# Optimization experiments

Hardware: AMD Instinct MI355X
Metric: run time of the kernel (lower is better)

## Reference

```python
import jax, jax.numpy as jnp
import numpy as np
import math

VOCAB = 128000
D_MODEL = 1024
CUTOFFS = [20000, 60000, VOCAB]  # cluster boundaries (last = vocab_size)
B, S = 8, 4096


def setup_inputs() -> dict:
    key = jax.random.key(0)
    ks = jax.random.split(key, 6)
    input_ids = jax.random.randint(ks[0], (B, S), 0, VOCAB)
    # cluster 0: ids [0, 20000), dim 1024, padding_idx=0 -> zero row
    emb0 = jax.random.normal(ks[1], (20000, 1024), jnp.float32)
    emb0 = emb0.at[0].set(0.0)
    # cluster 1: ids [20000, 60000), dim 256 (= 1024 // 4**1)
    emb1 = jax.random.normal(ks[2], (40000, 256), jnp.float32)
    # cluster 2: ids [60000, 128000), dim 64 (= 1024 // 4**2)
    emb2 = jax.random.normal(ks[3], (68000, 64), jnp.float32)
    # nn.Linear(emb_dim, d_model, bias=False): weight shape [d_model, emb_dim]
    proj1 = jax.random.normal(ks[4], (1024, 256), jnp.float32) * 0.02
    proj2 = jax.random.normal(ks[5], (1024, 64), jnp.float32) * 0.02
    return {"input_ids": input_ids, "emb0": emb0, "emb1": emb1, "emb2": emb2,
            "proj1": proj1, "proj2": proj2}


def reference(input_ids, emb0, emb1, emb2, proj1, proj2):
    d_model = emb0.shape[1]
    starts = [0, CUTOFFS[0], CUTOFFS[1]]
    ends = CUTOFFS
    tables = [emb0, emb1, emb2]
    projs = [None, proj1, proj2]
    out = jnp.zeros(input_ids.shape + (d_model,), jnp.float32)
    for start, end, tab, proj in zip(starts, ends, tables, projs):
        mask = (input_ids >= start) & (input_ids < end)          # [B,S]
        local = jnp.clip(input_ids - start, 0, tab.shape[0] - 1)  # in-range gather ids
        e = tab[local]                                            # [B,S,emb_dim]
        if proj is not None:
            e = jnp.einsum('bse,de->bsd', e, proj)                # project to d_model
        else:
            # padding_idx=0: row is zero; mask keeps grad out of row 0 too
            e = e * (input_ids != 0)[..., None].astype(e.dtype)
        out = out + jnp.where(mask[..., None], e, 0.0)            # masked scatter
    return out * math.sqrt(d_model)
```

## Files before the change

### kernel.cpp

```cpp
#include <hip/hip_runtime.h>
#include <hip/hip_bf16.h>


typedef __attribute__((ext_vector_type(4))) float        float4v;
typedef __attribute__((ext_vector_type(8))) short        short8;
typedef __attribute__((ext_vector_type(2))) unsigned int uint2v;
typedef __attribute__((ext_vector_type(2))) int          int2v;

#define D_MODEL 1024

__device__ __forceinline__ short f2bf(float x) {
    unsigned u = __builtin_bit_cast(unsigned, x);
    unsigned r = u + 0x7fffu + ((u >> 16) & 1u);
    return (short)(r >> 16);
}

__device__ __forceinline__ uint2v pack4(float4v v) {
    uint2v r;
    r[0] = (unsigned)(unsigned short)f2bf(v[0]) | ((unsigned)(unsigned short)f2bf(v[1]) << 16);
    r[1] = (unsigned)(unsigned short)f2bf(v[2]) | ((unsigned)(unsigned short)f2bf(v[3]) << 16);
    return r;
}

__global__ __launch_bounds__(1024)
void prep_k(const int* __restrict__ ids, int n, int pb,
            int* __restrict__ cnt,
            int2v* __restrict__ l0, int2v* __restrict__ l1, int2v* __restrict__ l2,
            const float* __restrict__ proj1, const float* __restrict__ proj2,
            uint2v* __restrict__ p1bf, uint2v* __restrict__ p2bf)
{
    const int b = blockIdx.x;
    if (b >= pb) {
        int bb = b - pb;
        if (bb < 64) {
            int t = bb * 1024 + threadIdx.x;
            p1bf[t] = pack4(((const float4v*)proj1)[t]);
        } else {
            int t = (bb - 64) * 1024 + threadIdx.x;
            p2bf[t] = pack4(((const float4v*)proj2)[t]);
        }
        return;
    }

    __shared__ int s_wcnt[16][3];
    __shared__ int s_wbase[16][3];
    __shared__ int s_base[3];

    const int tid  = threadIdx.x;
    const int wave = tid >> 6;
    const int lane = tid & 63;
    const int i    = b * 1024 + tid;

    int id = (i < n) ? ids[i] : -1;
    bool is0 = (i < n) && (id < 20000);
    bool is1 = (i < n) && (id >= 20000) && (id < 60000);
    bool is2 = (i < n) && (id >= 60000);
    unsigned long long ltmask = (lane == 0) ? 0ull : (~0ull >> (64 - lane));

    unsigned long long m0 = __ballot(is0);
    unsigned long long m1 = __ballot(is1);
    unsigned long long m2 = __ballot(is2);
    if (lane == 0) {
        s_wcnt[wave][0] = __popcll(m0);
        s_wcnt[wave][1] = __popcll(m1);
        s_wcnt[wave][2] = __popcll(m2);
    }
    __syncthreads();

    if (tid < 3) {
        const int c = tid;
        int run = 0;
#pragma unroll
        for (int w = 0; w < 16; w++) { s_wbase[w][c] = run; run += s_wcnt[w][c]; }
        const int gidx = (c == 0) ? 2 : (c - 1);
        s_base[c] = atomicAdd(&cnt[gidx], run);
    }
    __syncthreads();

    if (is0) l0[s_base[0] + s_wbase[wave][0] + __popcll(m0 & ltmask)] = (int2v){i, id};
    if (is1) l1[s_base[1] + s_wbase[wave][1] + __popcll(m1 & ltmask)] = (int2v){i, id - 20000};
    if (is2) l2[s_base[2] + s_wbase[wave][2] + __popcll(m2 & ltmask)] = (int2v){i, id - 60000};
}

template<int K>
__device__ __forceinline__
void gemm_item(int tile, int dimh,
               const float* __restrict__ table,
               const short* __restrict__ pbf,
               const int2v* __restrict__ list,
               int count,
               float* __restrict__ out,
               int2v* s_tl, short* s_a)
{
    constexpr int PK = K + 8;
    const int m_base = tile * 16;
    const int tid = threadIdx.x;
    if (tid < 16) {
        int m = m_base + tid;
        s_tl[tid] = (m < count) ? list[m] : (int2v){-1, 0};
    }
    __syncthreads();

    {
        const int row = tid >> 4;
        const int c   = tid & 15;
        const float* src = table + (size_t)s_tl[row][1] * K + c * (K / 16);
        short*       dst = s_a + row * PK + c * (K / 16);
        if constexpr (K == 256) {
            const float4v* s4 = (const float4v*)src;
            float4v f0 = s4[0], f1 = s4[1], f2 = s4[2], f3 = s4[3];
            uint2v* d2 = (uint2v*)dst;
            d2[0] = pack4(f0); d2[1] = pack4(f1);
            d2[2] = pack4(f2); d2[3] = pack4(f3);
        } else {
            float4v f0 = *(const float4v*)src;
            *(uint2v*)dst = pack4(f0);
        }
    }
    __syncthreads();

    const int lane = tid & 63;
    const int wave = tid >> 6;
    const int col  = lane & 15;
    const int quad = lane >> 4;
    const int nb   = dimh * 512 + wave * 128;

    const short* arow  = s_a + col * PK + quad * 8;
    const short* bbase = pbf + (size_t)(nb + col) * K + quad * 8;

    float4v acc[8];
#pragma unroll
    for (int i = 0; i < 8; i++) acc[i] = (float4v){0.f, 0.f, 0.f, 0.f};

#pragma unroll
    for (int ks = 0; ks < K; ks += 32) {
        short8 a = *(const short8*)(arow + ks);
#pragma unroll
        for (int nt = 0; nt < 8; nt++) {
            short8 b = *(const short8*)(bbase + (size_t)nt * 16 * K + ks);
            acc[nt] = __builtin_amdgcn_mfma_f32_16x16x32_bf16(a, b, acc[nt], 0, 0, 0);
        }
    }

#pragma unroll
    for (int r = 0; r < 4; r++) {
        int row = quad * 4 + r;
        if (m_base + row < count) {
            float* orow = out + (size_t)s_tl[row][0] * D_MODEL + nb + col;
#pragma unroll
            for (int nt = 0; nt < 8; nt++) orow[nt * 16] = acc[nt][r] * 32.0f;
        }
    }
    __syncthreads();
}

__device__ __forceinline__
void copy_item(int item, const int2v* __restrict__ l0, int count0,
               const float* __restrict__ emb0, float* __restrict__ out)
{
    int r = item * 4 + (threadIdx.x >> 6);
    if (r < count0) {
        int2v tl = l0[r];
        const float4v* src = (const float4v*)(emb0 + (size_t)tl[1] * D_MODEL);
        float4v*       dst = (float4v*)(out + (size_t)tl[0] * D_MODEL);
        int c = threadIdx.x & 63;
        float4v v0 = src[c], v1 = src[c + 64], v2 = src[c + 128], v3 = src[c + 192];
        dst[c]       = v0 * 32.0f;
        dst[c + 64]  = v1 * 32.0f;
        dst[c + 128] = v2 * 32.0f;
        dst[c + 192] = v3 * 32.0f;
    }
}

__global__ __launch_bounds__(256, 5)
void fused_main(const float* __restrict__ emb0,
                const float* __restrict__ emb1,
                const float* __restrict__ emb2,
                const short* __restrict__ p1bf,
                const short* __restrict__ p2bf,
                const int2v* __restrict__ l0,
                const int2v* __restrict__ l1,
                const int2v* __restrict__ l2,
                const int* __restrict__ cnt,
                float* __restrict__ out)
{
    __shared__ int2v s_tl[16];
    __shared__ short s_a[16 * 264];

    const int c1 = cnt[0];
    const int c2 = cnt[1];
    const int c0 = cnt[2];
    const int g1 = ((c1 + 15) >> 4) * 2;
    const int g2 = ((c2 + 15) >> 4) * 2;
    const int tc = (c0 + 3) >> 2;
    const int total = g1 + g2 + tc;

    for (int w = blockIdx.x; w < total; w += gridDim.x) {
        if (w < g1) {
            gemm_item<256>(w >> 1, w & 1, emb1, p1bf, l1, c1, out, s_tl, s_a);
        } else if (w < g1 + g2) {
            int u = w - g1;
            gemm_item<64>(u >> 1, u & 1, emb2, p2bf, l2, c2, out, s_tl, s_a);
        } else {
            copy_item(w - g1 - g2, l0, c0, emb0, out);
        }
    }
}

extern "C" void kernel_launch(void* const* d_in, const int* in_sizes, int n_in,
                              void* d_out, int out_size, void* d_ws, size_t ws_size,
                              hipStream_t stream)
{
    const int*   ids   = (const int*)  d_in[0];
    const float* emb0  = (const float*)d_in[1];
    const float* emb1  = (const float*)d_in[2];
    const float* emb2  = (const float*)d_in[3];
    const float* proj1 = (const float*)d_in[4];
    const float* proj2 = (const float*)d_in[5];
    float*       out   = (float*)d_out;
    const int n = in_sizes[0];

    int*   cnt  = (int*)d_ws;
    int2v* l0   = (int2v*)((char*)d_ws + 256);
    int2v* l1   = l0 + n;
    int2v* l2   = l1 + n;
    size_t poff = (256 + (size_t)3 * n * 8 + 255) & ~(size_t)255;
    short* p1bf = (short*)((char*)d_ws + poff);
    short* p2bf = p1bf + 1024 * 256;

    const int pb = (n + 1023) / 1024;

    hipMemsetAsync(cnt, 0, 4 * sizeof(int), stream);
    prep_k<<<pb + 64 + 16, 1024, 0, stream>>>(ids, n, pb, cnt, l0, l1, l2,
                                              proj1, proj2,
                                              (uint2v*)p1bf, (uint2v*)p2bf);
    fused_main<<<4096, 256, 0, stream>>>(emb0, emb1, emb2,
                                         p1bf, p2bf, l0, l1, l2, cnt, out);
}
```

Before: 289.4 us.

## Enlarge GEMM tiles to 32 rows, pre-swizzle projections, stage stores via LDS

The projection weights are now converted to bf16 in an MFMA-fragment order, so each lane loads one contiguous short8 per B fragment and the loads coalesce. Each 512-thread block now handles a 32-token tile across the full 1024-wide output, so two accumulator sets share every B fragment and the projection weights are re-read less often. Results are transposed through LDS so each row is written with float4 stores instead of scattered scalar stores. The cost is more registers and LDS per block (launch bounds change to 512 threads, 4 blocks) and extra barriers.

```diff
diff --git a/kernel.cpp b/kernel.cpp
--- a/kernel.cpp
+++ b/kernel.cpp
@@ -13,6 +13,13 @@
     unsigned u = __builtin_bit_cast(unsigned, x);
     unsigned r = u + 0x7fffu + ((u >> 16) & 1u);
     return (short)(r >> 16);
+}
+
+__device__ __forceinline__ short8 cvt8(float4v a, float4v b) {
+    short8 r;
+    r[0] = f2bf(a[0]); r[1] = f2bf(a[1]); r[2] = f2bf(a[2]); r[3] = f2bf(a[3]);
+    r[4] = f2bf(b[0]); r[5] = f2bf(b[1]); r[6] = f2bf(b[2]); r[7] = f2bf(b[3]);
+    return r;
 }
 
 __device__ __forceinline__ uint2v pack4(float4v v) {
@@ -27,17 +34,29 @@
             int* __restrict__ cnt,
             int2v* __restrict__ l0, int2v* __restrict__ l1, int2v* __restrict__ l2,
             const float* __restrict__ proj1, const float* __restrict__ proj2,
-            uint2v* __restrict__ p1bf, uint2v* __restrict__ p2bf)
+            short8* __restrict__ p1bf, short8* __restrict__ p2bf)
 {
     const int b = blockIdx.x;
     if (b >= pb) {
         int bb = b - pb;
-        if (bb < 64) {
-            int t = bb * 1024 + threadIdx.x;
-            p1bf[t] = pack4(((const float4v*)proj1)[t]);
+        if (bb < 32) {
+            int t    = bb * 1024 + threadIdx.x;
+            int lane = t & 63;
+            int ks32 = (t >> 6) & 7;
+            int nt   = t >> 9;
+            int nrow = nt * 16 + (lane & 15);
+            int k0   = ks32 * 32 + (lane >> 4) * 8;
+            const float* s = proj1 + nrow * 256 + k0;
+            p1bf[t] = cvt8(*(const float4v*)s, *(const float4v*)(s + 4));
         } else {
-            int t = (bb - 64) * 1024 + threadIdx.x;
-            p2bf[t] = pack4(((const float4v*)proj2)[t]);
+            int t    = (bb - 32) * 1024 + threadIdx.x;
+            int lane = t & 63;
+            int ks32 = (t >> 6) & 1;
+            int nt   = t >> 7;
+            int nrow = nt * 16 + (lane & 15);
+            int k0   = ks32 * 32 + (lane >> 4) * 8;
+            const float* s = proj2 + nrow * 64 + k0;
+            p2bf[t] = cvt8(*(const float4v*)s, *(const float4v*)(s + 4));
         }
         return;
     }
@@ -84,18 +103,19 @@
 
 template<int K>
 __device__ __forceinline__
-void gemm_item(int tile, int dimh,
+void gemm_tile(int tile,
                const float* __restrict__ table,
-               const short* __restrict__ pbf,
+               const short8* __restrict__ pbf,
                const int2v* __restrict__ list,
                int count,
                float* __restrict__ out,
-               int2v* s_tl, short* s_a)
+               int2v* s_tl, short* s_a, float* s_t)
 {
     constexpr int PK = K + 8;
-    const int m_base = tile * 16;
+    constexpr int KS = K / 32;
+    const int m_base = tile * 32;
     const int tid = threadIdx.x;
-    if (tid < 16) {
+    if (tid < 32) {
         int m = m_base + tid;
         s_tl[tid] = (m < count) ? list[m] : (int2v){-1, 0};
     }
@@ -104,7 +124,7 @@
     {
         const int row = tid >> 4;
         const int c   = tid & 15;
-        const float* src = table + (size_t)s_tl[row][1] * K + c * (K / 16);
+        const float* src = s_tl ? table + (size_t)s_tl[row][1] * K + c * (K / 16) : nullptr;
         short*       dst = s_a + row * PK + c * (K / 16);
         if constexpr (K == 256) {
             const float4v* s4 = (const float4v*)src;
@@ -123,32 +143,65 @@
     const int wave = tid >> 6;
     const int col  = lane & 15;
     const int quad = lane >> 4;
-    const int nb   = dimh * 512 + wave * 128;
-
-    const short* arow  = s_a + col * PK + quad * 8;
-    const short* bbase = pbf + (size_t)(nb + col) * K + quad * 8;
-
-    float4v acc[8];
-#pragma unroll
-    for (int i = 0; i < 8; i++) acc[i] = (float4v){0.f, 0.f, 0.f, 0.f};
-
-#pragma unroll
-    for (int ks = 0; ks < K; ks += 32) {
-        short8 a = *(const short8*)(arow + ks);
+
+    const short* arow0 = s_a + col * PK        + quad * 8;
+    const short* arow1 = s_a + (col + 16) * PK + quad * 8;
+
+    float4v acc0[8], acc1[8];
+#pragma unroll
+    for (int i = 0; i < 8; i++) {
+        acc0[i] = (float4v){0.f, 0.f, 0.f, 0.f};
+        acc1[i] = (float4v){0.f, 0.f, 0.f, 0.f};
+    }
+
+#pragma unroll
+    for (int ks32 = 0; ks32 < KS; ks32++) {
+        short8 a0 = *(const short8*)(arow0 + ks32 * 32);
+        short8 a1 = *(const short8*)(arow1 + ks32 * 32);
+        const short8* bp = pbf + ((size_t)(wave * 8) * KS + ks32) * 64 + lane;
 #pragma unroll
         for (int nt = 0; nt < 8; nt++) {
-            short8 b = *(const short8*)(bbase + (size_t)nt * 16 * K + ks);
-            acc[nt] = __builtin_amdgcn_mfma_f32_16x16x32_bf16(a, b, acc[nt], 0, 0, 0);
-        }
-    }
-
-#pragma unroll
-    for (int r = 0; r < 4; r++) {
-        int row = quad * 4 + r;
-        if (m_base + row < count) {
-            float* orow = out + (size_t)s_tl[row][0] * D_MODEL + nb + col;
-#pragma unroll
-            for (int nt = 0; nt < 8; nt++) orow[nt * 16] = acc[nt][r] * 32.0f;
+            short8 b = bp[(size_t)nt * KS * 64];
+            acc0[nt] = __builtin_amdgcn_mfma_f32_16x16x32_bf16(a0, b, acc0[nt], 0, 0, 0);
+            acc1[nt] = __builtin_amdgcn_mfma_f32_16x16x32_bf16(a1, b, acc1[nt], 0, 0, 0);
+        }
+    }
+
+    __syncthreads();
+    float* tsc = s_t + wave * (16 * 132);
+    const int c4 = (lane & 31) * 4;
+    const int half = lane >> 5;
+
+#pragma unroll
+    for (int nt = 0; nt < 8; nt++)
+#pragma unroll
+        for (int r = 0; r < 4; r++)
+            tsc[(quad * 4 + r) * 132 + nt * 16 + col] = acc0[nt][r] * 32.0f;
+    __syncthreads();
+#pragma unroll
+    for (int s = 0; s < 8; s++) {
+        int R = s * 2 + half;
+        float4v v = *(const float4v*)&tsc[R * 132 + c4];
+        if (m_base + R < count) {
+            int tok = s_tl[R][0];
+            *(float4v*)(out + (size_t)tok * D_MODEL + wave * 128 + c4) = v;
+        }
+    }
+    __syncthreads();
+
+#pragma unroll
+    for (int nt = 0; nt < 8; nt++)
+#pragma unroll
+        for (int r = 0; r < 4; r++)
+            tsc[(quad * 4 + r) * 132 + nt * 16 + col] = acc1[nt][r] * 32.0f;
+    __syncthreads();
+#pragma unroll
+    for (int s = 0; s < 8; s++) {
+        int R = s * 2 + half;
+        float4v v = *(const float4v*)&tsc[R * 132 + c4];
+        if (m_base + 16 + R < count) {
+            int tok = s_tl[16 + R][0];
+            *(float4v*)(out + (size_t)tok * D_MODEL + wave * 128 + c4) = v;
         }
     }
     __syncthreads();
@@ -158,7 +211,7 @@
 void copy_item(int item, const int2v* __restrict__ l0, int count0,
                const float* __restrict__ emb0, float* __restrict__ out)
 {
-    int r = item * 4 + (threadIdx.x >> 6);
+    int r = item * 8 + (threadIdx.x >> 6);
     if (r < count0) {
         int2v tl = l0[r];
         const float4v* src = (const float4v*)(emb0 + (size_t)tl[1] * D_MODEL);
@@ -172,37 +225,38 @@
     }
 }
 
-__global__ __launch_bounds__(256, 5)
+__global__ __launch_bounds__(512, 4)
 void fused_main(const float* __restrict__ emb0,
                 const float* __restrict__ emb1,
                 const float* __restrict__ emb2,
-                const short* __restrict__ p1bf,
-                const short* __restrict__ p2bf,
+                const short8* __restrict__ p1bf,
+                const short8* __restrict__ p2bf,
                 const int2v* __restrict__ l0,
                 const int2v* __restrict__ l1,
                 const int2v* __restrict__ l2,
                 const int* __restrict__ cnt,
                 float* __restrict__ out)
 {
-    __shared__ int2v s_tl[16];
-    __shared__ short s_a[16 * 264];
+    __shared__ int2v s_tl[32];
+    __shared__ char  s_buf[8 * 16 * 132 * 4];
+    short* s_a = (short*)s_buf;
+    float* s_t = (float*)s_buf;
 
     const int c1 = cnt[0];
     const int c2 = cnt[1];
     const int c0 = cnt[2];
-    const int g1 = ((c1 + 15) >> 4) * 2;
-    const int g2 = ((c2 + 15) >> 4) * 2;
-    const int tc = (c0 + 3) >> 2;
-    const int total = g1 + g2 + tc;
+    const int t1 = (c1 + 31) >> 5;
+    const int t2 = (c2 + 31) >> 5;
+    const int tc = (c0 + 7) >> 3;
+    const int total = t1 + t2 + tc;
 
     for (int w = blockIdx.x; w < total; w += gridDim.x) {
-        if (w < g1) {
-            gemm_item<256>(w >> 1, w & 1, emb1, p1bf, l1, c1, out, s_tl, s_a);
-        } else if (w < g1 + g2) {
-            int u = w - g1;
-            gemm_item<64>(u >> 1, u & 1, emb2, p2bf, l2, c2, out, s_tl, s_a);
+        if (w < t1) {
+            gemm_tile<256>(w, emb1, p1bf, l1, c1, out, s_tl, s_a, s_t);
+        } else if (w < t1 + t2) {
+            gemm_tile<64>(w - t1, emb2, p2bf, l2, c2, out, s_tl, s_a, s_t);
         } else {
-            copy_item(w - g1 - g2, l0, c0, emb0, out);
+            copy_item(w - t1 - t2, l0, c0, emb0, out);
         }
     }
 }
@@ -225,15 +279,14 @@
     int2v* l1   = l0 + n;
     int2v* l2   = l1 + n;
     size_t poff = (256 + (size_t)3 * n * 8 + 255) & ~(size_t)255;
-    short* p1bf = (short*)((char*)d_ws + poff);
-    short* p2bf = p1bf + 1024 * 256;
+    short8* p1bf = (short8*)((char*)d_ws + poff);
+    short8* p2bf = p1bf + 32768;
 
     const int pb = (n + 1023) / 1024;
 
     hipMemsetAsync(cnt, 0, 4 * sizeof(int), stream);
-    prep_k<<<pb + 64 + 16, 1024, 0, stream>>>(ids, n, pb, cnt, l0, l1, l2,
-                                              proj1, proj2,
-                                              (uint2v*)p1bf, (uint2v*)p2bf);
-    fused_main<<<4096, 256, 0, stream>>>(emb0, emb1, emb2,
+    prep_k<<<pb + 32 + 8, 1024, 0, stream>>>(ids, n, pb, cnt, l0, l1, l2,
+                                             proj1, proj2, p1bf, p2bf);
+    fused_main<<<2048, 512, 0, stream>>>(emb0, emb1, emb2,
                                          p1bf, p2bf, l0, l1, l2, cnt, out);
 }
```

Result: slower. 315.7 us (+9.1%).
